# Kernel tuning notes

Measured on AMD Instinct MI355X. Metric: run time of the kernel, lower is better.

The kernel has to match this reference:

```python
import jax, jax.numpy as jnp
import numpy as np

# ---- constants derived from module config ----
DEG_HIST = np.array([0., 12000., 20000., 13000., 4000., 1000.])
AVG_DEG_LOG = float((np.log(np.arange(len(DEG_HIST)) + 1.0) * DEG_HIST).sum() / DEG_HIST.sum())
N_NODES, N_EDGES, N_GRAPHS = 50000, 150000, 2000
D, E_D, TOWERS, F_OUT, N_LAYERS = 75, 50, 5, 15, 4
EPS = 1e-5


def setup_inputs() -> dict:
    key = jax.random.key(0)
    ks = jax.random.split(key, 16)
    g = lambda k, shape, s=0.05: (jax.random.normal(k, shape, jnp.float32) * s)
    return {
        'x': jax.random.randint(ks[0], (N_NODES,), 0, 21),
        'edge_index': jax.random.randint(ks[1], (2, N_EDGES), 0, N_NODES),
        'edge_attr': jax.random.randint(ks[2], (N_EDGES,), 0, 4),
        'batch': jnp.sort(jax.random.randint(ks[3], (N_NODES,), 0, N_GRAPHS)),
        'node_emb': g(ks[4], (21, D), 1.0),
        'edge_emb': g(ks[5], (4, E_D), 1.0),
        'We': g(ks[6], (N_LAYERS, E_D, D)),
        'be': jnp.zeros((N_LAYERS, D), jnp.float32),
        'Wpre': g(ks[7], (N_LAYERS, TOWERS, 3 * D, D)),
        'bpre': jnp.zeros((N_LAYERS, TOWERS, D), jnp.float32),
        'Wpost': g(ks[8], (N_LAYERS, TOWERS, 13 * D, F_OUT)),
        'bpost': jnp.zeros((N_LAYERS, TOWERS, F_OUT), jnp.float32),
        'Wlin': g(ks[9], (N_LAYERS, D, D)),
        'blin': jnp.zeros((N_LAYERS, D), jnp.float32),
        'gamma': jnp.ones((N_LAYERS, D), jnp.float32),
        'beta': jnp.zeros((N_LAYERS, D), jnp.float32),
        'W1': g(ks[10], (D, 50)), 'b1': jnp.zeros((50,), jnp.float32),
        'W2': g(ks[11], (50, 25)), 'b2': jnp.zeros((25,), jnp.float32),
        'W3': g(ks[12], (25, 1)), 'b3': jnp.zeros((1,), jnp.float32),
    }


def _pna_layer(x, src, dst, e_emb, We, be, Wpre, bpre, Wpost, bpost, Wlin, blin):
    # edge encoder (shared across towers)
    e = e_emb @ We + be                                        # [E, D]
    h = jnp.concatenate([x[dst], x[src], e], axis=-1)          # [E, 3D] = (x_i, x_j, e)
    m = jnp.einsum('ec,tcf->etf', h, Wpre) + bpre              # [E, T, D] per-tower pre_nn
    # multi-aggregator scatter (mean / min / max / std) onto target nodes
    deg = jax.ops.segment_sum(jnp.ones((src.shape[0],), x.dtype), dst, num_segments=N_NODES)
    denom = jnp.maximum(deg, 1.0)[:, None, None]
    mean = jax.ops.segment_sum(m, dst, num_segments=N_NODES) / denom
    mean_sq = jax.ops.segment_sum(m * m, dst, num_segments=N_NODES) / denom
    std = jnp.sqrt(jax.nn.relu(mean_sq - mean * mean) + 1e-5)
    has = (deg > 0)[:, None, None]
    mn = jnp.where(has, jax.ops.segment_min(m, dst, num_segments=N_NODES), 0.0)
    mx = jnp.where(has, jax.ops.segment_max(m, dst, num_segments=N_NODES), 0.0)
    agg = jnp.concatenate([mean, mn, mx, std], axis=-1)        # [N, T, 4D]
    # degree scalers: identity / amplification / attenuation
    amp = jnp.log(jnp.maximum(deg, 1.0) + 1.0)[:, None, None] / AVG_DEG_LOG
    out = jnp.concatenate([agg, agg * amp, agg / amp], axis=-1)  # [N, T, 12D]
    xt = jnp.broadcast_to(x[:, None, :], (x.shape[0], TOWERS, D))  # divide_input=False
    out = jnp.concatenate([xt, out], axis=-1)                   # [N, T, 13D]
    out = jnp.einsum('ntc,tcf->ntf', out, Wpost) + bpost        # [N, T, F_OUT] per-tower post_nn
    out = out.reshape(x.shape[0], TOWERS * F_OUT)               # [N, D]
    return out @ Wlin + blin


def _bn(x, gamma, beta):
    mu = x.mean(0)
    var = ((x - mu) ** 2).mean(0)  # biased, training-mode batch stats
    return gamma * (x - mu) / jnp.sqrt(var + EPS) + beta


def reference(x, edge_index, edge_attr, batch, node_emb, edge_emb, We, be, Wpre, bpre,
              Wpost, bpost, Wlin, blin, gamma, beta, W1, b1, W2, b2, W3, b3):
    src, dst = edge_index[0], edge_index[1]
    h = node_emb[x]                 # [N, 75]
    ea = edge_emb[edge_attr]        # [E, 50]
    for l in range(N_LAYERS):
        h = jax.nn.relu(_bn(_pna_layer(h, src, dst, ea, We[l], be[l], Wpre[l], bpre[l],
                                       Wpost[l], bpost[l], Wlin[l], blin[l]),
                            gamma[l], beta[l]))
    pooled = jax.ops.segment_sum(h, batch, num_segments=N_GRAPHS)  # global_add_pool
    z = jax.nn.relu(pooled @ W1 + b1)
    z = jax.nn.relu(z @ W2 + b2)
    return z @ W3 + b3  # [N_GRAPHS, 1]
```

## Files before the change

### kernel.cpp

```cpp
#include <hip/hip_runtime.h>
#include <math.h>

#define NN 50000
#define NE 150000
#define NG 2000
#define NL 4
#define AVG_DEG_LOG 1.1308269950720915f

typedef __attribute__((ext_vector_type(8))) short bf8_t;
typedef __attribute__((ext_vector_type(4))) float f4_t;

__device__ inline unsigned short f2bf(float x) {
  union { float f; unsigned int u; } v; v.f = x;
  unsigned int r = (v.u + 0x7FFFu + ((v.u >> 16) & 1u)) >> 16;
  return (unsigned short)r;
}
__device__ inline float bflo(unsigned int u) { union { unsigned int u; float f; } v; v.u = u << 16; return v.f; }
__device__ inline float bfhi(unsigned int u) { union { unsigned int u; float f; } v; v.u = u & 0xFFFF0000u; return v.f; }

__global__ void k_deg(const int* __restrict__ dst, int* __restrict__ deg) {
  int e = blockIdx.x * 256 + threadIdx.x;
  if (e < NE) atomicAdd(&deg[dst[e]], 1);
}

__global__ __launch_bounds__(1024) void k_scan(const int* __restrict__ deg, int* __restrict__ off) {
  __shared__ int wsum[16];
  __shared__ int wpre[16];
  __shared__ int carry_s;
  int tid = threadIdx.x, lane = tid & 63, wv = tid >> 6;
  if (tid == 0) carry_s = 0;
  __syncthreads();
  for (int base = 0; base < NN; base += 1024) {
    int i = base + tid;
    int v = (i < NN) ? deg[i] : 0;
    int incl = v;
    #pragma unroll
    for (int d = 1; d < 64; d <<= 1) { int t = __shfl_up(incl, d); if (lane >= d) incl += t; }
    if (lane == 63) wsum[wv] = incl;
    __syncthreads();
    if (wv == 0) {
      int s = (lane < 16) ? wsum[lane] : 0;
      int sc = s;
      #pragma unroll
      for (int d = 1; d < 16; d <<= 1) { int t = __shfl_up(sc, d); if (lane >= d) sc += t; }
      if (lane < 16) wpre[lane] = sc - s;
    }
    __syncthreads();
    int carry = carry_s;
    int excl = carry + wpre[wv] + incl - v;
    if (i < NN) off[i] = excl;
    __syncthreads();
    if (tid == 1023) carry_s = excl + v;
    __syncthreads();
  }
  if (tid == 0) off[NN] = carry_s;
}

__global__ void k_amp(const int* __restrict__ deg, const int* __restrict__ off,
                      float* __restrict__ amp, float* __restrict__ invamp, int* __restrict__ cursor) {
  int n = blockIdx.x * 256 + threadIdx.x;
  if (n < NN) {
    int d = deg[n]; if (d < 1) d = 1;
    float a = logf((float)d + 1.0f) / AVG_DEG_LOG;
    amp[n] = a; invamp[n] = 1.0f / a;
    cursor[n] = off[n];
  }
}

__global__ void k_fill(const int* __restrict__ src, const int* __restrict__ dst,
                       const int* __restrict__ attr, int* __restrict__ cursor,
                       unsigned int* __restrict__ cpack) {
  int e = blockIdx.x * 256 + threadIdx.x;
  if (e < NE) {
    int d = dst[e];
    int p = atomicAdd(&cursor[d], 1);
    cpack[p] = (unsigned int)src[e] | ((unsigned int)attr[e] << 16);
  }
}

__global__ void k_embed(const int* __restrict__ x, const float* __restrict__ emb, unsigned short* __restrict__ hbf) {
  int i = blockIdx.x * 256 + threadIdx.x;
  if (i < NN * 96) {
    int n = i / 96, c = i - (i / 96) * 96;
    hbf[i] = (c < 75) ? f2bf(emb[x[n] * 75 + c]) : (unsigned short)0;
  }
}

__global__ void k_wxlin(const float* __restrict__ Wpost, const float* __restrict__ Wlin, float* __restrict__ WXlin) {
  int l = blockIdx.x;
  for (int idx = threadIdx.x; idx < 5625; idx += 256) {
    int k = idx / 75, j = idx - (idx / 75) * 75;
    float s = 0.0f;
    for (int o = 0; o < 75; ++o) {
      int t = o / 15, jj = o - t * 15;
      s += Wpost[((l * 5 + t) * 975 + k) * 15 + jj] * Wlin[l * 5625 + o * 75 + j];
    }
    WXlin[l * 5625 + idx] = s;
  }
}

__global__ void k_zb(const float* __restrict__ bpost, const float* __restrict__ blin,
                     const float* __restrict__ Wlin, float* __restrict__ zb) {
  int l = blockIdx.x, j = threadIdx.x;
  if (j < 75) {
    float s = blin[l * 75 + j];
    for (int o = 0; o < 75; ++o) s += bpost[l * 75 + o] * Wlin[l * 5625 + o * 75 + j];
    zb[l * 75 + j] = s;
  }
}

__global__ void k_packB1(const float* __restrict__ Wpre, const float* __restrict__ WXlin,
                         unsigned short* __restrict__ B1T) {
  int idx = blockIdx.x * 256 + threadIdx.x;
  if (idx >= 4 * 896 * 96) return;
  int l = idx / (896 * 96); int rem = idx - l * (896 * 96);
  int c = rem / 96, k = rem - (rem / 96) * 96;
  float v = 0.0f;
  if (k < 75) {
    if (c < 375) {
      int t = c / 75, f = c - t * 75;
      v = Wpre[((l * 5 + t) * 225 + 75 + k) * 75 + f];
    } else if (c >= 384 && c < 759) {
      int o = c - 384; int t = o / 75, f = o - t * 75;
      v = Wpre[((l * 5 + t) * 225 + k) * 75 + f];
    } else if (c >= 759 && c < 834) {
      v = WXlin[l * 5625 + k * 75 + (c - 759)];
    }
  }
  B1T[idx] = f2bf(v);
}

__global__ void k_packWcomb(const float* __restrict__ Wpost, unsigned short* __restrict__ WcombT) {
  int idx = blockIdx.x * 256 + threadIdx.x;
  if (idx >= 4 * 5 * 48 * 320) return;
  int l = idx / (5 * 48 * 320); int rem = idx - l * (5 * 48 * 320);
  int t = rem / (48 * 320); rem -= t * (48 * 320);
  int j = rem / 320, k = rem - (rem / 320) * 320;
  float v = 0.0f;
  if (j < 45 && k < 300) {
    int s = j / 15, jj = j - s * 15;
    int f = k >> 2, agg = k & 3;
    v = Wpost[((l * 5 + t) * 975 + 75 + s * 300 + agg * 75 + f) * 15 + jj];
  }
  WcombT[idx] = f2bf(v);
}

__global__ void k_packWlin(const float* __restrict__ Wlin, unsigned short* __restrict__ WlinT) {
  int idx = blockIdx.x * 256 + threadIdx.x;
  if (idx >= 4 * 80 * 96) return;
  int l = idx / (80 * 96); int rem = idx - l * (80 * 96);
  int j = rem / 96, k = rem - (rem / 96) * 96;
  float v = (j < 75 && k < 75) ? Wlin[l * 5625 + k * 75 + j] : 0.0f;
  WlinT[idx] = f2bf(v);
}

__global__ void k_etab(const float* __restrict__ edge_emb, const float* __restrict__ We,
                       const float* __restrict__ be, const float* __restrict__ Wpre,
                       float* __restrict__ etab) {
  __shared__ float ev[75];
  int l = blockIdx.x >> 2, a = blockIdx.x & 3;
  int tid = threadIdx.x;
  if (tid < 75) {
    float acc = be[l * 75 + tid];
    for (int k = 0; k < 50; ++k) acc += edge_emb[a * 50 + k] * We[(l * 50 + k) * 75 + tid];
    ev[tid] = acc;
  }
  __syncthreads();
  for (int tf = tid; tf < 384; tf += 256) {
    float acc = 0.0f;
    if (tf < 375) {
      int t = tf / 75, f = tf - t * 75;
      for (int d = 0; d < 75; ++d) acc += ev[d] * Wpre[((l * 5 + t) * 225 + 150 + d) * 75 + f];
    }
    etab[(l * 4 + a) * 384 + tf] = acc;
  }
}

__global__ __launch_bounds__(256) void k_gemm1(const unsigned short* __restrict__ hbf,
                                               const unsigned short* __restrict__ B1T_l,
                                               const float* __restrict__ bpre_l,
                                               unsigned short* __restrict__ Hsrc,
                                               float* __restrict__ Cdst,
                                               float* __restrict__ Xpart) {
  int w = threadIdx.x >> 6, lane = threadIdx.x & 63;
  int l15 = lane & 15, l4 = lane >> 4;
  int m0 = blockIdx.y * 64 + w * 16;
  int n0 = blockIdx.x * 128;
  int mA = m0 + l15; if (mA >= NN) mA = NN - 1;
  bf8_t a0 = *(const bf8_t*)(hbf + (size_t)mA * 96 + l4 * 8);
  bf8_t a1 = *(const bf8_t*)(hbf + (size_t)mA * 96 + 32 + l4 * 8);
  bf8_t a2 = *(const bf8_t*)(hbf + (size_t)mA * 96 + 64 + l4 * 8);
  #pragma unroll
  for (int nf = 0; nf < 8; ++nf) {
    int c = n0 + nf * 16 + l15;
    const unsigned short* bp = B1T_l + (size_t)c * 96 + l4 * 8;
    f4_t acc = {0.f, 0.f, 0.f, 0.f};
    acc = __builtin_amdgcn_mfma_f32_16x16x32_bf16(a0, *(const bf8_t*)(bp), acc, 0, 0, 0);
    acc = __builtin_amdgcn_mfma_f32_16x16x32_bf16(a1, *(const bf8_t*)(bp + 32), acc, 0, 0, 0);
    acc = __builtin_amdgcn_mfma_f32_16x16x32_bf16(a2, *(const bf8_t*)(bp + 64), acc, 0, 0, 0);
    #pragma unroll
    for (int i = 0; i < 4; ++i) {
      int m = m0 + l4 * 4 + i;
      if (m < NN) {
        if (c < 384) Hsrc[(size_t)m * 384 + c] = f2bf(acc[i]);
        else if (c < 759) Cdst[(size_t)m * 375 + (c - 384)] = acc[i] + bpre_l[c - 384];
        else if (c < 834) Xpart[(size_t)m * 75 + (c - 759)] = acc[i];
      }
    }
  }
}

__global__ __launch_bounds__(256) void k_agg(const unsigned short* __restrict__ Hsrc,
                                             const float* __restrict__ Cdst,
                                             const int* __restrict__ off,
                                             const unsigned int* __restrict__ cpack,
                                             const float* __restrict__ etab_l,
                                             const unsigned short* __restrict__ WcombT_l,
                                             const unsigned short* __restrict__ WlinT_l,
                                             const float* __restrict__ amp,
                                             const float* __restrict__ invamp,
                                             const float* __restrict__ Xpart,
                                             const float* __restrict__ zb_l,
                                             float* __restrict__ Z) {
  __shared__ __align__(16) unsigned short A_s[8 * 1608];
  int tid = threadIdx.x;
  int w = tid >> 6, lane = tid & 63;
  int l15 = lane & 15, l4 = lane >> 4;
  int n0 = blockIdx.x * 8;

  for (int idx = tid; idx < 400; idx += 256) {
    int n = idx / 50; int r = idx - n * 50; int t = r / 10; int j = r - t * 10;
    *((unsigned int*)&A_s[n * 1608 + t * 320 + 300] + j) = 0u;
  }

  int c0 = lane * 6;
  int lane3 = lane * 3;
  for (int r = 0; r < 2; ++r) {
    int nl = w * 2 + r;
    int g = n0 + nl;
    int e0 = off[g], e1 = off[g + 1];
    float s6[6] = {0,0,0,0,0,0}, q6[6] = {0,0,0,0,0,0};
    float mn6[6], mx6[6];
    #pragma unroll
    for (int i = 0; i < 6; ++i) { mn6[i] = 3.402823466e+38f; mx6[i] = -3.402823466e+38f; }
    for (int e = e0; e < e1; ++e) {
      unsigned int pk = cpack[e];
      unsigned int sidx = pk & 0xFFFFu;
      unsigned int a = pk >> 16;
      const unsigned int* hp = (const unsigned int*)Hsrc + (size_t)sidx * 192 + lane3;
      unsigned int u0 = hp[0], u1 = hp[1], u2 = hp[2];
      const float2* ep = (const float2*)(etab_l + a * 384 + c0);
      float2 ea = ep[0], eb = ep[1], ec = ep[2];
      float v[6] = { bflo(u0), bfhi(u0), bflo(u1), bfhi(u1), bflo(u2), bfhi(u2) };
      float ee[6] = { ea.x, ea.y, eb.x, eb.y, ec.x, ec.y };
      #pragma unroll
      for (int i = 0; i < 6; ++i) {
        float q = v[i] + ee[i];
        s6[i] += q;
        q6[i] = fmaf(q, q, q6[i]);
        mn6[i] = fminf(mn6[i], q);
        mx6[i] = fmaxf(mx6[i], q);
      }
    }
    int d = e1 - e0;
    float inv = (d > 0) ? (1.0f / (float)d) : 0.0f;
    #pragma unroll
    for (int i = 0; i < 6; ++i) {
      int c = c0 + i;
      if (c < 375) {
        float mean, mnv, mxv, sd;
        if (d > 0) {
          float cd = Cdst[(size_t)g * 375 + c];
          float mu = s6[i] * inv;
          mean = cd + mu;
          mnv = cd + mn6[i];
          mxv = cd + mx6[i];
          sd = sqrtf(fmaxf(q6[i] * inv - mu * mu, 0.0f) + 1e-5f);
        } else { mean = 0.0f; mnv = 0.0f; mxv = 0.0f; sd = 0.0031622776601683794f; }
        int t = c / 75, f = c - t * 75;
        uint2 pk2;
        pk2.x = (unsigned int)f2bf(mean) | ((unsigned int)f2bf(mnv) << 16);
        pk2.y = (unsigned int)f2bf(mxv) | ((unsigned int)f2bf(sd) << 16);
        *(uint2*)&A_s[nl * 1608 + t * 320 + f * 4] = pk2;
      }
    }
  }
  __syncthreads();

  f4_t accs[4];
  #pragma unroll
  for (int r = 0; r < 4; ++r) {
    int task = w + r * 4;
    f4_t acc = {0.f, 0.f, 0.f, 0.f};
    if (task < 15) {
      int t = task % 5, nf = task / 5;
      const unsigned short* ap = &A_s[(l15 & 7) * 1608 + t * 320 + l4 * 8];
      const unsigned short* wp = WcombT_l + (size_t)(t * 48 + nf * 16 + l15) * 320 + l4 * 8;
      #pragma unroll
      for (int ks = 0; ks < 10; ++ks) {
        bf8_t av = *(const bf8_t*)(ap + ks * 32);
        bf8_t bv = *(const bf8_t*)(wp + ks * 32);
        acc = __builtin_amdgcn_mfma_f32_16x16x32_bf16(av, bv, acc, 0, 0, 0);
      }
    }
    accs[r] = acc;
  }
  __syncthreads();

  float* Out = (float*)A_s;
  #pragma unroll
  for (int r = 0; r < 4; ++r) {
    int task = w + r * 4;
    if (task < 15) {
      int t = task % 5, nf = task / 5;
      #pragma unroll
      for (int i = 0; i < 4; ++i) {
        int row = l4 * 4 + i;
        if (row < 8) Out[row * 256 + t * 48 + nf * 16 + l15] = accs[r][i];
      }
    }
  }
  __syncthreads();

  unsigned short* Cb = (unsigned short*)((char*)A_s + 8192);
  for (int item = tid; item < 8 * 104; item += 256) {
    int n = item / 104, o = item - (item / 104) * 104;
    unsigned short v = 0;
    if (o < 75) {
      int t = o / 15, jj = o - (o / 15) * 15;
      int g = n0 + n;
      const float* ob = Out + n * 256 + t * 48;
      float cv = ob[jj] + amp[g] * ob[15 + jj] + invamp[g] * ob[30 + jj];
      v = f2bf(cv);
    }
    Cb[n * 104 + o] = v;
  }
  __syncthreads();

  #pragma unroll
  for (int r = 0; r < 2; ++r) {
    int nf = w + r * 4;
    if (nf < 5) {
      int cc = nf * 16 + l15;
      f4_t acc = {0.f, 0.f, 0.f, 0.f};
      const unsigned short* ap2 = Cb + (l15 & 7) * 104;
      const unsigned short* bp2 = WlinT_l + (size_t)cc * 96;
      #pragma unroll
      for (int ks = 0; ks < 3; ++ks) {
        bf8_t av = *(const bf8_t*)(ap2 + ks * 32 + l4 * 8);
        bf8_t bv = *(const bf8_t*)(bp2 + ks * 32 + l4 * 8);
        acc = __builtin_amdgcn_mfma_f32_16x16x32_bf16(av, bv, acc, 0, 0, 0);
      }
      if (cc < 75) {
        #pragma unroll
        for (int i = 0; i < 4; ++i) {
          int row = l4 * 4 + i;
          if (row < 8) {
            int g = n0 + row;
            Z[(size_t)g * 75 + cc] = acc[i] + Xpart[(size_t)g * 75 + cc] + zb_l[cc];
          }
        }
      }
    }
  }
}

#define BN_BLOCKS 256
#define BN_ROWS 196
__global__ __launch_bounds__(256) void k_bnstats(const float* __restrict__ Z, float* __restrict__ partial) {
  __shared__ float sArr[225];
  __shared__ float qArr[225];
  int tid = threadIdx.x;
  int r0 = blockIdx.x * BN_ROWS;
  int r1 = r0 + BN_ROWS; if (r1 > NN) r1 = NN;
  float s = 0.0f, q = 0.0f;
  if (tid < 225) {
    int rr = tid / 75, c = tid - rr * 75;
    for (int r = r0 + rr; r < r1; r += 3) {
      float v = Z[(size_t)r * 75 + c];
      s += v; q += v * v;
    }
    sArr[tid] = s; qArr[tid] = q;
  }
  __syncthreads();
  if (tid < 75) {
    float S = sArr[tid] + sArr[75 + tid] + sArr[150 + tid];
    float Q = qArr[tid] + qArr[75 + tid] + qArr[150 + tid];
    partial[blockIdx.x * 150 + tid] = S;
    partial[blockIdx.x * 150 + 75 + tid] = Q;
  }
}

__global__ void k_bnfinal(const float* __restrict__ partial, float* __restrict__ musig) {
  int c = threadIdx.x;
  if (c < 75) {
    float S = 0.0f, Q = 0.0f;
    for (int b = 0; b < BN_BLOCKS; ++b) { S += partial[b * 150 + c]; Q += partial[b * 150 + 75 + c]; }
    float mu = S * (1.0f / NN);
    float var = fmaxf(Q * (1.0f / NN) - mu * mu, 0.0f);
    musig[c] = mu;
    musig[75 + c] = 1.0f / sqrtf(var + 1e-5f);
  }
}

__global__ void k_bnapply(const float* __restrict__ Z, const float* __restrict__ musig,
                          const float* __restrict__ gamma_l, const float* __restrict__ beta_l,
                          unsigned short* __restrict__ hbf, float* __restrict__ hf32, int last) {
  int i = blockIdx.x * 256 + threadIdx.x;
  if (i < NN * 96) {
    int n = i / 96, c = i - (i / 96) * 96;
    if (c < 75) {
      float v = (Z[(size_t)n * 75 + c] - musig[c]) * musig[75 + c];
      v = fmaxf(gamma_l[c] * v + beta_l[c], 0.0f);
      if (last) hf32[(size_t)n * 75 + c] = v;
      else hbf[i] = f2bf(v);
    } else if (!last) {
      hbf[i] = 0;
    }
  }
}

__global__ __launch_bounds__(128) void k_pool_mlp(const float* __restrict__ h, const int* __restrict__ batch,
                                                  const float* __restrict__ W1, const float* __restrict__ b1,
                                                  const float* __restrict__ W2, const float* __restrict__ b2,
                                                  const float* __restrict__ W3, const float* __restrict__ b3,
                                                  float* __restrict__ out) {
  __shared__ float pooled[75];
  __shared__ float z1[50];
  __shared__ float z2[25];
  __shared__ int se[2];
  int g = blockIdx.x, tid = threadIdx.x;
  if (tid < 2) {
    int target = g + tid;
    int lo = 0, hi = NN;
    while (lo < hi) { int mid = (lo + hi) >> 1; if (batch[mid] < target) lo = mid + 1; else hi = mid; }
    se[tid] = lo;
  }
  __syncthreads();
  int s = se[0], e = se[1];
  if (tid < 75) {
    float acc = 0.0f;
    for (int r = s; r < e; ++r) acc += h[(size_t)r * 75 + tid];
    pooled[tid] = acc;
  }
  __syncthreads();
  if (tid < 50) {
    float acc = b1[tid];
    for (int c = 0; c < 75; ++c) acc += pooled[c] * W1[c * 50 + tid];
    z1[tid] = fmaxf(acc, 0.0f);
  }
  __syncthreads();
  if (tid < 25) {
    float acc = b2[tid];
    for (int c = 0; c < 50; ++c) acc += z1[c] * W2[c * 25 + tid];
    z2[tid] = fmaxf(acc, 0.0f);
  }
  __syncthreads();
  if (tid == 0) {
    float acc = b3[0];
    for (int c = 0; c < 25; ++c) acc += z2[c] * W3[c];
    out[g] = acc;
  }
}

extern "C" void kernel_launch(void* const* d_in, const int* in_sizes, int n_in,
                              void* d_out, int out_size, void* d_ws, size_t ws_size,
                              hipStream_t stream) {
  const int* x = (const int*)d_in[0];
  const int* ei = (const int*)d_in[1];
  const int* eattr = (const int*)d_in[2];
  const int* batch = (const int*)d_in[3];
  const float* node_emb = (const float*)d_in[4];
  const float* edge_emb = (const float*)d_in[5];
  const float* We = (const float*)d_in[6];
  const float* be = (const float*)d_in[7];
  const float* Wpre = (const float*)d_in[8];
  const float* bpre = (const float*)d_in[9];
  const float* Wpost = (const float*)d_in[10];
  const float* bpost = (const float*)d_in[11];
  const float* Wlin = (const float*)d_in[12];
  const float* blin = (const float*)d_in[13];
  const float* gamma = (const float*)d_in[14];
  const float* beta = (const float*)d_in[15];
  const float* W1 = (const float*)d_in[16];
  const float* b1 = (const float*)d_in[17];
  const float* W2 = (const float*)d_in[18];
  const float* b2 = (const float*)d_in[19];
  const float* W3 = (const float*)d_in[20];
  const float* b3 = (const float*)d_in[21];
  float* out = (float*)d_out;

  const int* src = ei;
  const int* dst = ei + NE;

  char* p = (char*)d_ws;
  auto alloc = [&](size_t bytes) { char* r = p; p += (bytes + 255) & ~(size_t)255; return r; };
  int* deg     = (int*)alloc((size_t)NN * 4);
  int* off     = (int*)alloc((size_t)(NN + 1) * 4);
  int* cursor  = (int*)alloc((size_t)NN * 4);
  unsigned int* cpack = (unsigned int*)alloc((size_t)NE * 4);
  float* amp    = (float*)alloc((size_t)NN * 4);
  float* invamp = (float*)alloc((size_t)NN * 4);
  unsigned short* hbf  = (unsigned short*)alloc((size_t)NN * 96 * 2);
  float* hf32          = (float*)alloc((size_t)NN * 75 * 4);
  unsigned short* Hsrc = (unsigned short*)alloc((size_t)NN * 384 * 2);
  float* Cdst          = (float*)alloc((size_t)NN * 375 * 4);
  float* Xpart         = (float*)alloc((size_t)NN * 75 * 4);
  float* Z             = (float*)alloc((size_t)NN * 75 * 4);
  unsigned short* B1T    = (unsigned short*)alloc((size_t)4 * 896 * 96 * 2);
  unsigned short* WcombT = (unsigned short*)alloc((size_t)4 * 5 * 48 * 320 * 2);
  unsigned short* WlinT  = (unsigned short*)alloc((size_t)4 * 80 * 96 * 2);
  float* WXlin = (float*)alloc((size_t)4 * 5625 * 4);
  float* zb    = (float*)alloc((size_t)4 * 75 * 4);
  float* etab  = (float*)alloc((size_t)4 * 4 * 384 * 4);
  float* bnpart = (float*)alloc((size_t)BN_BLOCKS * 150 * 4);
  float* musig  = (float*)alloc((size_t)150 * 4);

  hipMemsetAsync(deg, 0, (size_t)NN * 4, stream);
  k_deg<<<(NE + 255) / 256, 256, 0, stream>>>(dst, deg);
  k_scan<<<1, 1024, 0, stream>>>(deg, off);
  k_amp<<<(NN + 255) / 256, 256, 0, stream>>>(deg, off, amp, invamp, cursor);
  k_fill<<<(NE + 255) / 256, 256, 0, stream>>>(src, dst, eattr, cursor, cpack);
  k_embed<<<(NN * 96 + 255) / 256, 256, 0, stream>>>(x, node_emb, hbf);
  k_wxlin<<<4, 256, 0, stream>>>(Wpost, Wlin, WXlin);
  k_zb<<<4, 128, 0, stream>>>(bpost, blin, Wlin, zb);
  k_packB1<<<(4 * 896 * 96 + 255) / 256, 256, 0, stream>>>(Wpre, WXlin, B1T);
  k_packWcomb<<<(4 * 5 * 48 * 320 + 255) / 256, 256, 0, stream>>>(Wpost, WcombT);
  k_packWlin<<<(4 * 80 * 96 + 255) / 256, 256, 0, stream>>>(Wlin, WlinT);
  k_etab<<<16, 256, 0, stream>>>(edge_emb, We, be, Wpre, etab);

  dim3 g1(7, (NN + 63) / 64);
  for (int l = 0; l < NL; ++l) {
    k_gemm1<<<g1, 256, 0, stream>>>(hbf, B1T + (size_t)l * 896 * 96, bpre + l * 375, Hsrc, Cdst, Xpart);
    k_agg<<<NN / 8, 256, 0, stream>>>(Hsrc, Cdst, off, cpack,
                                      etab + (size_t)l * 4 * 384,
                                      WcombT + (size_t)l * 5 * 48 * 320,
                                      WlinT + (size_t)l * 80 * 96,
                                      amp, invamp, Xpart, zb + l * 75, Z);
    k_bnstats<<<BN_BLOCKS, 256, 0, stream>>>(Z, bnpart);
    k_bnfinal<<<1, 128, 0, stream>>>(bnpart, musig);
    k_bnapply<<<(NN * 96 + 255) / 256, 256, 0, stream>>>(Z, musig, gamma + l * 75, beta + l * 75, hbf, hf32, l == NL - 1);
  }
  k_pool_mlp<<<NG, 128, 0, stream>>>(hf32, batch, W1, b1, W2, b2, W3, b3, out);
}
```

Before: 1.324 ms.

## Fuse destination-side and Xlin projections into aggregation kernel, widen to 512 threads

The destination-node projection (Cdst with bias) and the skip projection (Xpart) are no longer computed by the first GEMM and written to global memory. The aggregation kernel now recomputes them per block with MFMA into shared memory. That kernel also moves to 512 threads with one wave per node, 8-wide bf16 gathers unrolled over 4 edges, and the edge table staged in shared memory. This removes large fp32 intermediate round trips, at the cost of more shared memory and higher per-block register pressure.

```diff
diff --git a/kernel.cpp b/kernel.cpp
--- a/kernel.cpp
+++ b/kernel.cpp
@@ -109,25 +109,47 @@
   }
 }
 
-__global__ void k_packB1(const float* __restrict__ Wpre, const float* __restrict__ WXlin,
-                         unsigned short* __restrict__ B1T) {
+__global__ void k_packAll(const float* __restrict__ Wpre, const float* __restrict__ WXlin,
+                          const float* __restrict__ Wlin,
+                          unsigned short* __restrict__ B1Ts, unsigned short* __restrict__ B1Td,
+                          unsigned short* __restrict__ WXT, unsigned short* __restrict__ WlinT) {
+  const int S1 = 4 * 384 * 96;
+  const int S2 = S1 + 4 * 384 * 96;
+  const int S3 = S2 + 4 * 80 * 96;
+  const int S4 = S3 + 4 * 80 * 96;
   int idx = blockIdx.x * 256 + threadIdx.x;
-  if (idx >= 4 * 896 * 96) return;
-  int l = idx / (896 * 96); int rem = idx - l * (896 * 96);
-  int c = rem / 96, k = rem - (rem / 96) * 96;
-  float v = 0.0f;
-  if (k < 75) {
-    if (c < 375) {
+  if (idx < S1) {
+    int l = idx / (384 * 96); int rem = idx - l * (384 * 96);
+    int c = rem / 96, k = rem - (rem / 96) * 96;
+    float v = 0.0f;
+    if (c < 375 && k < 75) {
       int t = c / 75, f = c - t * 75;
       v = Wpre[((l * 5 + t) * 225 + 75 + k) * 75 + f];
-    } else if (c >= 384 && c < 759) {
-      int o = c - 384; int t = o / 75, f = o - t * 75;
+    }
+    B1Ts[idx] = f2bf(v);
+  } else if (idx < S2) {
+    int m = idx - S1;
+    int l = m / (384 * 96); int rem = m - l * (384 * 96);
+    int c = rem / 96, k = rem - (rem / 96) * 96;
+    float v = 0.0f;
+    if (c < 375 && k < 75) {
+      int t = c / 75, f = c - t * 75;
       v = Wpre[((l * 5 + t) * 225 + k) * 75 + f];
-    } else if (c >= 759 && c < 834) {
-      v = WXlin[l * 5625 + k * 75 + (c - 759)];
-    }
-  }
-  B1T[idx] = f2bf(v);
+    }
+    B1Td[m] = f2bf(v);
+  } else if (idx < S3) {
+    int m = idx - S2;
+    int l = m / (80 * 96); int rem = m - l * (80 * 96);
+    int j = rem / 96, k = rem - (rem / 96) * 96;
+    float v = (j < 75 && k < 75) ? WXlin[l * 5625 + k * 75 + j] : 0.0f;
+    WXT[m] = f2bf(v);
+  } else if (idx < S4) {
+    int m = idx - S3;
+    int l = m / (80 * 96); int rem = m - l * (80 * 96);
+    int j = rem / 96, k = rem - (rem / 96) * 96;
+    float v = (j < 75 && k < 75) ? Wlin[l * 5625 + k * 75 + j] : 0.0f;
+    WlinT[m] = f2bf(v);
+  }
 }
 
 __global__ void k_packWcomb(const float* __restrict__ Wpost, unsigned short* __restrict__ WcombT) {
@@ -145,15 +167,6 @@
   WcombT[idx] = f2bf(v);
 }
 
-__global__ void k_packWlin(const float* __restrict__ Wlin, unsigned short* __restrict__ WlinT) {
-  int idx = blockIdx.x * 256 + threadIdx.x;
-  if (idx >= 4 * 80 * 96) return;
-  int l = idx / (80 * 96); int rem = idx - l * (80 * 96);
-  int j = rem / 96, k = rem - (rem / 96) * 96;
-  float v = (j < 75 && k < 75) ? Wlin[l * 5625 + k * 75 + j] : 0.0f;
-  WlinT[idx] = f2bf(v);
-}
-
 __global__ void k_etab(const float* __restrict__ edge_emb, const float* __restrict__ We,
                        const float* __restrict__ be, const float* __restrict__ Wpre,
                        float* __restrict__ etab) {
@@ -177,23 +190,19 @@
 }
 
 __global__ __launch_bounds__(256) void k_gemm1(const unsigned short* __restrict__ hbf,
-                                               const unsigned short* __restrict__ B1T_l,
-                                               const float* __restrict__ bpre_l,
-                                               unsigned short* __restrict__ Hsrc,
-                                               float* __restrict__ Cdst,
-                                               float* __restrict__ Xpart) {
+                                               const unsigned short* __restrict__ B1Ts_l,
+                                               unsigned short* __restrict__ Hsrc) {
   int w = threadIdx.x >> 6, lane = threadIdx.x & 63;
   int l15 = lane & 15, l4 = lane >> 4;
-  int m0 = blockIdx.y * 64 + w * 16;
-  int n0 = blockIdx.x * 128;
+  int m0 = blockIdx.x * 64 + w * 16;
   int mA = m0 + l15; if (mA >= NN) mA = NN - 1;
-  bf8_t a0 = *(const bf8_t*)(hbf + (size_t)mA * 96 + l4 * 8);
-  bf8_t a1 = *(const bf8_t*)(hbf + (size_t)mA * 96 + 32 + l4 * 8);
-  bf8_t a2 = *(const bf8_t*)(hbf + (size_t)mA * 96 + 64 + l4 * 8);
-  #pragma unroll
-  for (int nf = 0; nf < 8; ++nf) {
-    int c = n0 + nf * 16 + l15;
-    const unsigned short* bp = B1T_l + (size_t)c * 96 + l4 * 8;
+  const unsigned short* ha = hbf + (size_t)mA * 96 + l4 * 8;
+  bf8_t a0 = *(const bf8_t*)(ha);
+  bf8_t a1 = *(const bf8_t*)(ha + 32);
+  bf8_t a2 = *(const bf8_t*)(ha + 64);
+  for (int nf = 0; nf < 24; ++nf) {
+    int c = nf * 16 + l15;
+    const unsigned short* bp = B1Ts_l + (size_t)c * 96 + l4 * 8;
     f4_t acc = {0.f, 0.f, 0.f, 0.f};
     acc = __builtin_amdgcn_mfma_f32_16x16x32_bf16(a0, *(const bf8_t*)(bp), acc, 0, 0, 0);
     acc = __builtin_amdgcn_mfma_f32_16x16x32_bf16(a1, *(const bf8_t*)(bp + 32), acc, 0, 0, 0);
@@ -201,96 +210,157 @@
     #pragma unroll
     for (int i = 0; i < 4; ++i) {
       int m = m0 + l4 * 4 + i;
-      if (m < NN) {
-        if (c < 384) Hsrc[(size_t)m * 384 + c] = f2bf(acc[i]);
-        else if (c < 759) Cdst[(size_t)m * 375 + (c - 384)] = acc[i] + bpre_l[c - 384];
-        else if (c < 834) Xpart[(size_t)m * 75 + (c - 759)] = acc[i];
-      }
-    }
-  }
-}
-
-__global__ __launch_bounds__(256) void k_agg(const unsigned short* __restrict__ Hsrc,
-                                             const float* __restrict__ Cdst,
-                                             const int* __restrict__ off,
-                                             const unsigned int* __restrict__ cpack,
-                                             const float* __restrict__ etab_l,
-                                             const unsigned short* __restrict__ WcombT_l,
-                                             const unsigned short* __restrict__ WlinT_l,
-                                             const float* __restrict__ amp,
-                                             const float* __restrict__ invamp,
-                                             const float* __restrict__ Xpart,
-                                             const float* __restrict__ zb_l,
-                                             float* __restrict__ Z) {
+      if (m < NN) Hsrc[(size_t)m * 384 + c] = f2bf(acc[i]);
+    }
+  }
+}
+
+__global__ __launch_bounds__(512, 4) void k_agg(
+    const unsigned short* __restrict__ hbf,
+    const unsigned short* __restrict__ Hsrc,
+    const int* __restrict__ off,
+    const unsigned int* __restrict__ cpack,
+    const float* __restrict__ etab_l,
+    const unsigned short* __restrict__ B1Td_l,
+    const float* __restrict__ bpre_l,
+    const unsigned short* __restrict__ WXT_l,
+    const unsigned short* __restrict__ WcombT_l,
+    const unsigned short* __restrict__ WlinT_l,
+    const float* __restrict__ amp,
+    const float* __restrict__ invamp,
+    const float* __restrict__ zb_l,
+    float* __restrict__ Z) {
   __shared__ __align__(16) unsigned short A_s[8 * 1608];
+  __shared__ __align__(16) float Cd_s[8 * 384];
+  __shared__ __align__(16) float Xp_s[8 * 80];
+  __shared__ __align__(16) float et_s[4 * 384];
   int tid = threadIdx.x;
   int w = tid >> 6, lane = tid & 63;
   int l15 = lane & 15, l4 = lane >> 4;
   int n0 = blockIdx.x * 8;
 
-  for (int idx = tid; idx < 400; idx += 256) {
+  for (int i = tid; i < 1536; i += 512) et_s[i] = etab_l[i];
+  for (int idx = tid; idx < 400; idx += 512) {
     int n = idx / 50; int r = idx - n * 50; int t = r / 10; int j = r - t * 10;
     *((unsigned int*)&A_s[n * 1608 + t * 320 + 300] + j) = 0u;
   }
 
-  int c0 = lane * 6;
-  int lane3 = lane * 3;
+  {
+    int arow = n0 + (l15 & 7);
+    const unsigned short* ha = hbf + (size_t)arow * 96 + l4 * 8;
+    bf8_t pa0 = *(const bf8_t*)(ha);
+    bf8_t pa1 = *(const bf8_t*)(ha + 32);
+    bf8_t pa2 = *(const bf8_t*)(ha + 64);
+    #pragma unroll
+    for (int r = 0; r < 3; ++r) {
+      int c = (w + r * 8) * 16 + l15;
+      const unsigned short* bp = B1Td_l + (size_t)c * 96 + l4 * 8;
+      f4_t acc = {0.f, 0.f, 0.f, 0.f};
+      acc = __builtin_amdgcn_mfma_f32_16x16x32_bf16(pa0, *(const bf8_t*)(bp), acc, 0, 0, 0);
+      acc = __builtin_amdgcn_mfma_f32_16x16x32_bf16(pa1, *(const bf8_t*)(bp + 32), acc, 0, 0, 0);
+      acc = __builtin_amdgcn_mfma_f32_16x16x32_bf16(pa2, *(const bf8_t*)(bp + 64), acc, 0, 0, 0);
+      float bb = (c < 375) ? bpre_l[c] : 0.0f;
+      #pragma unroll
+      for (int i = 0; i < 4; ++i) {
+        int row = l4 * 4 + i;
+        if (row < 8) Cd_s[row * 384 + c] = acc[i] + bb;
+      }
+    }
+    if (w < 5) {
+      int c = w * 16 + l15;
+      const unsigned short* bp = WXT_l + (size_t)c * 96 + l4 * 8;
+      f4_t acc = {0.f, 0.f, 0.f, 0.f};
+      acc = __builtin_amdgcn_mfma_f32_16x16x32_bf16(pa0, *(const bf8_t*)(bp), acc, 0, 0, 0);
+      acc = __builtin_amdgcn_mfma_f32_16x16x32_bf16(pa1, *(const bf8_t*)(bp + 32), acc, 0, 0, 0);
+      acc = __builtin_amdgcn_mfma_f32_16x16x32_bf16(pa2, *(const bf8_t*)(bp + 64), acc, 0, 0, 0);
+      #pragma unroll
+      for (int i = 0; i < 4; ++i) {
+        int row = l4 * 4 + i;
+        if (row < 8) Xp_s[row * 80 + c] = acc[i];
+      }
+    }
+  }
+  __syncthreads();
+
+  {
+    int g = n0 + w;
+    int e0 = off[g], e1 = off[g + 1];
+    if (lane < 47) {
+      int c0 = lane * 8;
+      float s8[8], q8[8], mn8[8], mx8[8];
+      #pragma unroll
+      for (int j = 0; j < 8; ++j) {
+        s8[j] = 0.0f; q8[j] = 0.0f;
+        mn8[j] = 3.402823466e+38f; mx8[j] = -3.402823466e+38f;
+      }
+      auto acc8 = [&](bf8_t hv, unsigned int aa) {
+        union { bf8_t v; unsigned int u[4]; } cv; cv.v = hv;
+        const float* ep = &et_s[aa * 384 + c0];
+        f4_t ea = *(const f4_t*)ep;
+        f4_t eb = *(const f4_t*)(ep + 4);
+        float vv[8], ee[8];
+        #pragma unroll
+        for (int j = 0; j < 4; ++j) {
+          vv[2 * j] = bflo(cv.u[j]); vv[2 * j + 1] = bfhi(cv.u[j]);
+          ee[j] = ea[j]; ee[4 + j] = eb[j];
+        }
+        #pragma unroll
+        for (int j = 0; j < 8; ++j) {
+          float q = vv[j] + ee[j];
+          s8[j] += q;
+          q8[j] = fmaf(q, q, q8[j]);
+          mn8[j] = fminf(mn8[j], q);
+          mx8[j] = fmaxf(mx8[j], q);
+        }
+      };
+      for (int e = e0; e < e1; ) {
+        int m = e1 - e;
+        unsigned int pk0 = cpack[e];
+        unsigned int pk1 = cpack[m > 1 ? e + 1 : e];
+        unsigned int pk2 = cpack[m > 2 ? e + 2 : e];
+        unsigned int pk3 = cpack[m > 3 ? e + 3 : e];
+        bf8_t h0 = *((const bf8_t*)(Hsrc + (size_t)(pk0 & 0xFFFFu) * 384) + lane);
+        bf8_t h1 = *((const bf8_t*)(Hsrc + (size_t)(pk1 & 0xFFFFu) * 384) + lane);
+        bf8_t h2 = *((const bf8_t*)(Hsrc + (size_t)(pk2 & 0xFFFFu) * 384) + lane);
+        bf8_t h3 = *((const bf8_t*)(Hsrc + (size_t)(pk3 & 0xFFFFu) * 384) + lane);
+        acc8(h0, pk0 >> 16);
+        if (m > 1) acc8(h1, pk1 >> 16);
+        if (m > 2) acc8(h2, pk2 >> 16);
+        if (m > 3) acc8(h3, pk3 >> 16);
+        e += (m < 4) ? m : 4;
+      }
+      int d = e1 - e0;
+      float inv = (d > 0) ? (1.0f / (float)d) : 0.0f;
+      f4_t cda = *(const f4_t*)&Cd_s[w * 384 + c0];
+      f4_t cdb = *(const f4_t*)&Cd_s[w * 384 + c0 + 4];
+      #pragma unroll
+      for (int j = 0; j < 8; ++j) {
+        int c = c0 + j;
+        if (c < 375) {
+          float cd = (j < 4) ? cda[j] : cdb[j - 4];
+          float mean, mnv, mxv, sd;
+          if (d > 0) {
+            float mu = s8[j] * inv;
+            mean = cd + mu;
+            mnv = cd + mn8[j];
+            mxv = cd + mx8[j];
+            sd = sqrtf(fmaxf(q8[j] * inv - mu * mu, 0.0f) + 1e-5f);
+          } else { mean = 0.0f; mnv = 0.0f; mxv = 0.0f; sd = 0.0031622776601683794f; }
+          int t = c / 75, f = c - (c / 75) * 75;
+          uint2 pkv;
+          pkv.x = (unsigned int)f2bf(mean) | ((unsigned int)f2bf(mnv) << 16);
+          pkv.y = (unsigned int)f2bf(mxv) | ((unsigned int)f2bf(sd) << 16);
+          *(uint2*)&A_s[w * 1608 + t * 320 + f * 4] = pkv;
+        }
+      }
+    }
+  }
+  __syncthreads();
+
+  f4_t accs[2];
+  #pragma unroll
   for (int r = 0; r < 2; ++r) {
-    int nl = w * 2 + r;
-    int g = n0 + nl;
-    int e0 = off[g], e1 = off[g + 1];
-    float s6[6] = {0,0,0,0,0,0}, q6[6] = {0,0,0,0,0,0};
-    float mn6[6], mx6[6];
-    #pragma unroll
-    for (int i = 0; i < 6; ++i) { mn6[i] = 3.402823466e+38f; mx6[i] = -3.402823466e+38f; }
-    for (int e = e0; e < e1; ++e) {
-      unsigned int pk = cpack[e];
-      unsigned int sidx = pk & 0xFFFFu;
-      unsigned int a = pk >> 16;
-      const unsigned int* hp = (const unsigned int*)Hsrc + (size_t)sidx * 192 + lane3;
-      unsigned int u0 = hp[0], u1 = hp[1], u2 = hp[2];
-      const float2* ep = (const float2*)(etab_l + a * 384 + c0);
-      float2 ea = ep[0], eb = ep[1], ec = ep[2];
-      float v[6] = { bflo(u0), bfhi(u0), bflo(u1), bfhi(u1), bflo(u2), bfhi(u2) };
-      float ee[6] = { ea.x, ea.y, eb.x, eb.y, ec.x, ec.y };
-      #pragma unroll
-      for (int i = 0; i < 6; ++i) {
-        float q = v[i] + ee[i];
-        s6[i] += q;
-        q6[i] = fmaf(q, q, q6[i]);
-        mn6[i] = fminf(mn6[i], q);
-        mx6[i] = fmaxf(mx6[i], q);
-      }
-    }
-    int d = e1 - e0;
-    float inv = (d > 0) ? (1.0f / (float)d) : 0.0f;
-    #pragma unroll
-    for (int i = 0; i < 6; ++i) {
-      int c = c0 + i;
-      if (c < 375) {
-        float mean, mnv, mxv, sd;
-        if (d > 0) {
-          float cd = Cdst[(size_t)g * 375 + c];
-          float mu = s6[i] * inv;
-          mean = cd + mu;
-          mnv = cd + mn6[i];
-          mxv = cd + mx6[i];
-          sd = sqrtf(fmaxf(q6[i] * inv - mu * mu, 0.0f) + 1e-5f);
-        } else { mean = 0.0f; mnv = 0.0f; mxv = 0.0f; sd = 0.0031622776601683794f; }
-        int t = c / 75, f = c - t * 75;
-        uint2 pk2;
-        pk2.x = (unsigned int)f2bf(mean) | ((unsigned int)f2bf(mnv) << 16);
-        pk2.y = (unsigned int)f2bf(mxv) | ((unsigned int)f2bf(sd) << 16);
-        *(uint2*)&A_s[nl * 1608 + t * 320 + f * 4] = pk2;
-      }
-    }
-  }
-  __syncthreads();
-
-  f4_t accs[4];
-  #pragma unroll
-  for (int r = 0; r < 4; ++r) {
-    int task = w + r * 4;
+    int task = w + r * 8;
     f4_t acc = {0.f, 0.f, 0.f, 0.f};
     if (task < 15) {
       int t = task % 5, nf = task / 5;
@@ -309,8 +379,8 @@
 
   float* Out = (float*)A_s;
   #pragma unroll
-  for (int r = 0; r < 4; ++r) {
-    int task = w + r * 4;
+  for (int r = 0; r < 2; ++r) {
+    int task = w + r * 8;
     if (task < 15) {
       int t = task % 5, nf = task / 5;
       #pragma unroll
@@ -323,7 +393,7 @@
   __syncthreads();
 
   unsigned short* Cb = (unsigned short*)((char*)A_s + 8192);
-  for (int item = tid; item < 8 * 104; item += 256) {
+  for (int item = tid; item < 8 * 104; item += 512) {
     int n = item / 104, o = item - (item / 104) * 104;
     unsigned short v = 0;
     if (o < 75) {
@@ -337,28 +407,24 @@
   }
   __syncthreads();
 
-  #pragma unroll
-  for (int r = 0; r < 2; ++r) {
-    int nf = w + r * 4;
-    if (nf < 5) {
-      int cc = nf * 16 + l15;
-      f4_t acc = {0.f, 0.f, 0.f, 0.f};
-      const unsigned short* ap2 = Cb + (l15 & 7) * 104;
-      const unsigned short* bp2 = WlinT_l + (size_t)cc * 96;
-      #pragma unroll
-      for (int ks = 0; ks < 3; ++ks) {
-        bf8_t av = *(const bf8_t*)(ap2 + ks * 32 + l4 * 8);
-        bf8_t bv = *(const bf8_t*)(bp2 + ks * 32 + l4 * 8);
-        acc = __builtin_amdgcn_mfma_f32_16x16x32_bf16(av, bv, acc, 0, 0, 0);
-      }
-      if (cc < 75) {
-        #pragma unroll
-        for (int i = 0; i < 4; ++i) {
-          int row = l4 * 4 + i;
-          if (row < 8) {
-            int g = n0 + row;
-            Z[(size_t)g * 75 + cc] = acc[i] + Xpart[(size_t)g * 75 + cc] + zb_l[cc];
-          }
+  if (w < 5) {
+    int cc = w * 16 + l15;
+    f4_t acc = {0.f, 0.f, 0.f, 0.f};
+    const unsigned short* ap2 = Cb + (l15 & 7) * 104;
+    const unsigned short* bp2 = WlinT_l + (size_t)cc * 96;
+    #pragma unroll
+    for (int ks = 0; ks < 3; ++ks) {
+      bf8_t av = *(const bf8_t*)(ap2 + ks * 32 + l4 * 8);
+      bf8_t bv = *(const bf8_t*)(bp2 + ks * 32 + l4 * 8);
+      acc = __builtin_amdgcn_mfma_f32_16x16x32_bf16(av, bv, acc, 0, 0, 0);
+    }
+    if (cc < 75) {
+      #pragma unroll
+      for (int i = 0; i < 4; ++i) {
+        int row = l4 * 4 + i;
+        if (row < 8) {
+          int g = n0 + row;
+          Z[(size_t)g * 75 + cc] = acc[i] + Xp_s[row * 80 + cc] + zb_l[cc];
         }
       }
     }
@@ -503,13 +569,13 @@
   float* invamp = (float*)alloc((size_t)NN * 4);
   unsigned short* hbf  = (unsigned short*)alloc((size_t)NN * 96 * 2);
   float* hf32          = (float*)alloc((size_t)NN * 75 * 4);
-  unsigned short* Hsrc = (unsigned short*)alloc((size_t)NN * 384 * 2);
-  float* Cdst          = (float*)alloc((size_t)NN * 375 * 4);
-  float* Xpart         = (float*)alloc((size_t)NN * 75 * 4);
-  float* Z             = (float*)alloc((size_t)NN * 75 * 4);
-  unsigned short* B1T    = (unsigned short*)alloc((size_t)4 * 896 * 96 * 2);
+  unsigned short* Hsrc = (unsigned short*)alloc((size_t)NN * 384 * 2 + 256);
+  float* Z             = (float*)alloc((size_t)NN * 75 * 4 + 256);
+  unsigned short* B1Ts   = (unsigned short*)alloc((size_t)4 * 384 * 96 * 2);
+  unsigned short* B1Td   = (unsigned short*)alloc((size_t)4 * 384 * 96 * 2);
+  unsigned short* WXT    = (unsigned short*)alloc((size_t)4 * 80 * 96 * 2);
+  unsigned short* WlinT  = (unsigned short*)alloc((size_t)4 * 80 * 96 * 2);
   unsigned short* WcombT = (unsigned short*)alloc((size_t)4 * 5 * 48 * 320 * 2);
-  unsigned short* WlinT  = (unsigned short*)alloc((size_t)4 * 80 * 96 * 2);
   float* WXlin = (float*)alloc((size_t)4 * 5625 * 4);
   float* zb    = (float*)alloc((size_t)4 * 75 * 4);
   float* etab  = (float*)alloc((size_t)4 * 4 * 384 * 4);
@@ -524,19 +590,23 @@
   k_embed<<<(NN * 96 + 255) / 256, 256, 0, stream>>>(x, node_emb, hbf);
   k_wxlin<<<4, 256, 0, stream>>>(Wpost, Wlin, WXlin);
   k_zb<<<4, 128, 0, stream>>>(bpost, blin, Wlin, zb);
-  k_packB1<<<(4 * 896 * 96 + 255) / 256, 256, 0, stream>>>(Wpre, WXlin, B1T);
+  {
+    int tot = 4 * 384 * 96 * 2 + 4 * 80 * 96 * 2;
+    k_packAll<<<(tot + 255) / 256, 256, 0, stream>>>(Wpre, WXlin, Wlin, B1Ts, B1Td, WXT, WlinT);
+  }
   k_packWcomb<<<(4 * 5 * 48 * 320 + 255) / 256, 256, 0, stream>>>(Wpost, WcombT);
-  k_packWlin<<<(4 * 80 * 96 + 255) / 256, 256, 0, stream>>>(Wlin, WlinT);
   k_etab<<<16, 256, 0, stream>>>(edge_emb, We, be, Wpre, etab);
 
-  dim3 g1(7, (NN + 63) / 64);
   for (int l = 0; l < NL; ++l) {
-    k_gemm1<<<g1, 256, 0, stream>>>(hbf, B1T + (size_t)l * 896 * 96, bpre + l * 375, Hsrc, Cdst, Xpart);
-    k_agg<<<NN / 8, 256, 0, stream>>>(Hsrc, Cdst, off, cpack,
+    k_gemm1<<<(NN + 63) / 64, 256, 0, stream>>>(hbf, B1Ts + (size_t)l * 384 * 96, Hsrc);
+    k_agg<<<NN / 8, 512, 0, stream>>>(hbf, Hsrc, off, cpack,
                                       etab + (size_t)l * 4 * 384,
+                                      B1Td + (size_t)l * 384 * 96,
+                                      bpre + l * 375,
+                                      WXT + (size_t)l * 80 * 96,
                                       WcombT + (size_t)l * 5 * 48 * 320,
                                       WlinT + (size_t)l * 80 * 96,
-                                      amp, invamp, Xpart, zb + l * 75, Z);
+                                      amp, invamp, zb + l * 75, Z);
     k_bnstats<<<BN_BLOCKS, 256, 0, stream>>>(Z, bnpart);
     k_bnfinal<<<1, 128, 0, stream>>>(bnpart, musig);
     k_bnapply<<<(NN * 96 + 255) / 256, 256, 0, stream>>>(Z, musig, gamma + l * 75, beta + l * 75, hbf, hf32, l == NL - 1);
```

Result: slower. 1.412 ms (+6.6%).
